# Performance work log

Measured on AMD Instinct MI355X. Metric: run time of the kernel, lower is better.

Reference implementation:

```python
import jax, jax.numpy as jnp
from jax import lax
import numpy as np

V = 50000          # num_word; embedding table has V+1 rows
D = 512            # embedding_dim / d_model
H = 8              # nhead
FF = 2048          # dim_feedforward (hidden_dim)
L = 32             # num_label (incl START/STOP)
START, STOP = L - 2, L - 1
S = 2048           # sentence length
NEG = -10000.0


def setup_inputs() -> dict:
    k = jax.random.split(jax.random.key(0), 10)
    def rn(key, shape, s=0.02):
        return jax.random.normal(key, shape, jnp.float32) * s
    transitions = jax.random.normal(k[8], (L, L), jnp.float32)
    transitions = transitions.at[START, :].set(NEG).at[:, STOP].set(NEG)
    return {
        "sentence": jax.random.randint(k[0], (S,), 0, V + 1),
        "embed": rn(k[1], (V + 1, D), 1.0),
        "Wqkv": rn(k[2], (3 * D, D)), "bqkv": jnp.zeros((3 * D,), jnp.float32),
        "Wo": rn(k[3], (D, D)), "bo": jnp.zeros((D,), jnp.float32),
        "ln1_g": jnp.ones((D,), jnp.float32), "ln1_b": jnp.zeros((D,), jnp.float32),
        "W1": rn(k[4], (FF, D)), "b1": jnp.zeros((FF,), jnp.float32),
        "W2": rn(k[5], (D, FF)), "b2": jnp.zeros((D,), jnp.float32),
        "ln2_g": jnp.ones((D,), jnp.float32), "ln2_b": jnp.zeros((D,), jnp.float32),
        "Wt": rn(k[6], (L, D)), "bt": jnp.zeros((L,), jnp.float32),
        "transitions": transitions,
    }


def _ln(x, g, b):
    m = jnp.mean(x, -1, keepdims=True)
    v = jnp.var(x, -1, keepdims=True)
    return (x - m) * lax.rsqrt(v + 1e-5) * g + b


def _transformer_feats(sentence, embed, Wqkv, bqkv, Wo, bo, ln1_g, ln1_b,
                       W1, b1, W2, b2, ln2_g, ln2_b, Wt, bt):
    x = embed[sentence]                                   # [S, D]
    qkv = x @ Wqkv.T + bqkv                               # [S, 3D]
    q, k, v = jnp.split(qkv, 3, axis=-1)
    to_heads = lambda t: t.reshape(S, H, D // H).transpose(1, 0, 2)  # [H, S, dh]
    q, k, v = to_heads(q), to_heads(k), to_heads(v)
    att = jax.nn.softmax(jnp.einsum('hsd,htd->hst', q, k) / np.float32(np.sqrt(D // H)), axis=-1)
    o = jnp.einsum('hst,htd->hsd', att, v).transpose(1, 0, 2).reshape(S, D)
    # post-norm TransformerEncoderLayer (eval mode: dropout off), relu FFN
    x = _ln(x + o @ Wo.T + bo, ln1_g, ln1_b)
    ff = jax.nn.relu(x @ W1.T + b1) @ W2.T + b2
    x = _ln(x + ff, ln2_g, ln2_b)
    return x @ Wt.T + bt                                  # [S, L] emission scores


def _viterbi(feats, transitions):
    init = jnp.full((L,), NEG, jnp.float32).at[START].set(0.0)
    def step(prev, emit):
        scores = prev[None, :] + transitions              # [next_tag, prev_tag]
        bp = jnp.argmax(scores, axis=1)                   # best prev tag per next tag
        return jnp.max(scores, axis=1) + emit, bp
    last, bps = lax.scan(step, init, feats)               # bps: [S, L]
    terminal = last + transitions[STOP]
    best = jnp.argmax(terminal)
    def back(tag, bp):
        return bp[tag], tag
    _, path = lax.scan(back, best, bps, reverse=True)     # path[t] = best tag at step t
    return terminal[best], path


def reference(sentence, embed, Wqkv, bqkv, Wo, bo, ln1_g, ln1_b,
              W1, b1, W2, b2, ln2_g, ln2_b, Wt, bt, transitions):
    feats = _transformer_feats(sentence, embed, Wqkv, bqkv, Wo, bo, ln1_g, ln1_b,
                               W1, b1, W2, b2, ln2_g, ln2_b, Wt, bt)
    score, path = _viterbi(feats, transitions)
    return score, path
```

## Files before the change

kernel.cpp:

```cpp
#include <hip/hip_runtime.h>
#include <cstddef>

#define S_LEN 2048
#define D_MODEL 512
#define NHEAD 8
#define DH 64
#define FF_DIM 2048
#define L_TAGS 32
#define START_TAG 30
#define STOP_TAG 31
#define NEGV (-10000.0f)

typedef unsigned int uint2v __attribute__((ext_vector_type(2)));
typedef __attribute__((ext_vector_type(8))) short short8v;
typedef __attribute__((ext_vector_type(4))) float f32x4;

union U8 { uint4 u; short8v s; };

__device__ __forceinline__ unsigned short f2bf(float f) {
  unsigned u = __float_as_uint(f);
  u += 0x7fff + ((u >> 16) & 1);
  return (unsigned short)(u >> 16);
}
__device__ __forceinline__ unsigned cvtpk(float lo, float hi) {
  unsigned r;
  asm("v_cvt_pk_bf16_f32 %0, %1, %2" : "=v"(r) : "v"(lo), "v"(hi));
  return r;
}

__global__ __launch_bounds__(256) void k_f2h4(const float* __restrict__ s0, short* __restrict__ d0,
                                              const float* __restrict__ s1, short* __restrict__ d1,
                                              const float* __restrict__ s2, short* __restrict__ d2,
                                              const float* __restrict__ s3, short* __restrict__ d3) {
  const int b = blockIdx.x;
  const float* src; short* dst; int i;
  if (b < 384)       { src = s0; dst = d0; i = b * 256 + threadIdx.x; }
  else if (b < 512)  { src = s1; dst = d1; i = (b - 384) * 256 + threadIdx.x; }
  else if (b < 1024) { src = s2; dst = d2; i = (b - 512) * 256 + threadIdx.x; }
  else               { src = s3; dst = d3; i = (b - 1024) * 256 + threadIdx.x; }
  f32x4 a = *(const f32x4*)(src + (size_t)i * 8);
  f32x4 c = *(const f32x4*)(src + (size_t)i * 8 + 4);
  U8 t;
  t.u.x = cvtpk(a[0], a[1]); t.u.y = cvtpk(a[2], a[3]);
  t.u.z = cvtpk(c[0], c[1]); t.u.w = cvtpk(c[2], c[3]);
  *(short8v*)(dst + (size_t)i * 8) = t.s;
}

__global__ __launch_bounds__(256, 2) void k_gemm_qkv(const int* __restrict__ sent,
                                                     const float* __restrict__ embed,
                                                     const short* __restrict__ B,
                                                     const float* __restrict__ bias,
                                                     short* __restrict__ C,
                                                     int N, int K) {
  __shared__ __align__(16) short As[2][128 * 64];
  __shared__ __align__(16) short Bs[2][128 * 64];
  const int tid = threadIdx.x;
  const int bm = blockIdx.y * 128, bn = blockIdx.x * 128;
  const int w = tid >> 6, lane = tid & 63;
  const int wr = w >> 1, wc = w & 1;
  const int fr = lane & 15, kg = lane >> 4;
  const int srow = tid >> 1, sc0 = (tid & 1) * 4;
  const int swz = srow & 7;
  const float* gA = embed + (size_t)sent[bm + srow] * K + sc0 * 8;
  const short* gB = B + (size_t)(bn + srow) * K + sc0 * 8;
  f32x4 ra[8];
  short8v rb[4];
  f32x4 acc[4][4] = {};

  auto loadg = [&](int k0) {
#pragma unroll
    for (int c = 0; c < 4; ++c) {
      ra[2 * c] = *(const f32x4*)(gA + k0 + c * 8);
      ra[2 * c + 1] = *(const f32x4*)(gA + k0 + c * 8 + 4);
      rb[c] = *(const short8v*)(gB + k0 + c * 8);
    }
  };
  auto storeb = [&](int b) {
    short* dA = &As[b][srow * 64];
    short* dB = &Bs[b][srow * 64];
#pragma unroll
    for (int c = 0; c < 4; ++c) {
      U8 ta;
      ta.u.x = cvtpk(ra[2 * c][0], ra[2 * c][1]);
      ta.u.y = cvtpk(ra[2 * c][2], ra[2 * c][3]);
      ta.u.z = cvtpk(ra[2 * c + 1][0], ra[2 * c + 1][1]);
      ta.u.w = cvtpk(ra[2 * c + 1][2], ra[2 * c + 1][3]);
      *(short8v*)(dA + (((sc0 + c) ^ swz) << 3)) = ta.s;
      *(short8v*)(dB + (((sc0 + c) ^ swz) << 3)) = rb[c];
    }
  };

  loadg(0);
  storeb(0);
  __syncthreads();
  int cur = 0;
  const int fswz = fr & 7;
  for (int k0 = 0; k0 < K; k0 += 64) {
    const bool more = (k0 + 64) < K;
    if (more) loadg(k0 + 64);
    const short* rA = &As[cur][(wr * 64 + fr) * 64];
    const short* rB = &Bs[cur][(wc * 64 + fr) * 64];
#pragma unroll
    for (int ks = 0; ks < 2; ++ks) {
      const int co = ((ks * 4 + kg) ^ fswz) << 3;
      short8v af[4], bf[4];
#pragma unroll
      for (int rt = 0; rt < 4; ++rt) af[rt] = *(const short8v*)(rA + rt * 16 * 64 + co);
#pragma unroll
      for (int ct = 0; ct < 4; ++ct) bf[ct] = *(const short8v*)(rB + ct * 16 * 64 + co);
#pragma unroll
      for (int rt = 0; rt < 4; ++rt)
#pragma unroll
        for (int ct = 0; ct < 4; ++ct)
          acc[rt][ct] = __builtin_amdgcn_mfma_f32_16x16x32_bf16(af[rt], bf[ct], acc[rt][ct], 0, 0, 0);
    }
    if (more) storeb(cur ^ 1);
    __syncthreads();
    cur ^= 1;
  }
#pragma unroll
  for (int rt = 0; rt < 4; ++rt) {
#pragma unroll
    for (int ct = 0; ct < 4; ++ct) {
      f32x4 v = acc[rt][ct];
      const int row0 = bm + wr * 64 + rt * 16 + kg * 4;
      const int col = bn + wc * 64 + ct * 16 + fr;
      const float bs = bias[col];
#pragma unroll
      for (int j = 0; j < 4; ++j)
        C[(size_t)(row0 + j) * N + col] = (short)f2bf(v[j] + bs);
    }
  }
}

template <int RT, bool RELU, bool OBF>
__global__ __launch_bounds__(256, 2) void k_gemm_bf(const short* __restrict__ A,
                                                    const short* __restrict__ B,
                                                    const float* __restrict__ bias,
                                                    void* __restrict__ Cp,
                                                    int M, int N, int K) {
  constexpr int BM = RT * 32;
  constexpr int CH = (BM * 8) / 256;
  __shared__ __align__(16) short As[2][BM * 64];
  __shared__ __align__(16) short Bs[2][BM * 64];
  const int tid = threadIdx.x;
  const int bm = blockIdx.y * BM, bn = blockIdx.x * BM;
  const int w = tid >> 6, lane = tid & 63;
  const int wr = w >> 1, wc = w & 1;
  const int fr = lane & 15, kg = lane >> 4;
  const int srow = (RT == 4) ? (tid >> 1) : (tid >> 2);
  const int sc0 = (RT == 4) ? ((tid & 1) * 4) : ((tid & 3) * 2);
  const int swz = srow & 7;
  const short* gA = A + (size_t)(bm + srow) * K + sc0 * 8;
  const short* gB = B + (size_t)(bn + srow) * K + sc0 * 8;
  short8v ra[CH], rb[CH];
  f32x4 acc[RT][RT] = {};

  auto loadg = [&](int k0) {
#pragma unroll
    for (int c = 0; c < CH; ++c) {
      ra[c] = *(const short8v*)(gA + k0 + c * 8);
      rb[c] = *(const short8v*)(gB + k0 + c * 8);
    }
  };
  auto storeb = [&](int b) {
    short* dA = &As[b][srow * 64];
    short* dB = &Bs[b][srow * 64];
#pragma unroll
    for (int c = 0; c < CH; ++c) {
      *(short8v*)(dA + (((sc0 + c) ^ swz) << 3)) = ra[c];
      *(short8v*)(dB + (((sc0 + c) ^ swz) << 3)) = rb[c];
    }
  };

  loadg(0);
  storeb(0);
  __syncthreads();
  int cur = 0;
  const int fswz = fr & 7;
  for (int k0 = 0; k0 < K; k0 += 64) {
    const bool more = (k0 + 64) < K;
    if (more) loadg(k0 + 64);
    const short* rA = &As[cur][(wr * (RT * 16) + fr) * 64];
    const short* rB = &Bs[cur][(wc * (RT * 16) + fr) * 64];
#pragma unroll
    for (int ks = 0; ks < 2; ++ks) {
      const int co = ((ks * 4 + kg) ^ fswz) << 3;
      short8v af[RT], bf[RT];
#pragma unroll
      for (int rt = 0; rt < RT; ++rt) af[rt] = *(const short8v*)(rA + rt * 16 * 64 + co);
#pragma unroll
      for (int ct = 0; ct < RT; ++ct) bf[ct] = *(const short8v*)(rB + ct * 16 * 64 + co);
#pragma unroll
      for (int rt = 0; rt < RT; ++rt)
#pragma unroll
        for (int ct = 0; ct < RT; ++ct)
          acc[rt][ct] = __builtin_amdgcn_mfma_f32_16x16x32_bf16(af[rt], bf[ct], acc[rt][ct], 0, 0, 0);
    }
    if (more) storeb(cur ^ 1);
    __syncthreads();
    cur ^= 1;
  }
#pragma unroll
  for (int rt = 0; rt < RT; ++rt) {
#pragma unroll
    for (int ct = 0; ct < RT; ++ct) {
      f32x4 v = acc[rt][ct];
      const int row0 = bm + wr * (RT * 16) + rt * 16 + kg * 4;
      const int col = bn + wc * (RT * 16) + ct * 16 + fr;
      const float bs = bias[col];
#pragma unroll
      for (int j = 0; j < 4; ++j) {
        float o = v[j] + bs;
        if (RELU) o = fmaxf(o, 0.f);
        if (OBF)
          ((short*)Cp)[(size_t)(row0 + j) * N + col] = (short)f2bf(o);
        else
          ((float*)Cp)[(size_t)(row0 + j) * N + col] = o;
      }
    }
  }
}

__global__ __launch_bounds__(256) void k_attn(const short* __restrict__ qkv,
                                              short* __restrict__ ob) {
  __shared__ __align__(16) short Ks[2][64 * 64];
  __shared__ __align__(16) short Vt[2][64 * 72];
  __shared__ __align__(16) short Pl[4][16 * 72];
  const int tid = threadIdx.x;
  const int b = blockIdx.x;
  const int h = b & 7;
  const int bq = (b >> 3) * 64;
  const int wq = tid >> 6, lane = tid & 63;
  const int fr = lane & 15, kg = lane >> 4;
  short8v qf[2];
  {
    const short* qsrc = qkv + (size_t)(bq + wq * 16 + fr) * 1536 + h * DH;
    qf[0] = *(const short8v*)(qsrc + kg * 8);
    qf[1] = *(const short8v*)(qsrc + 32 + kg * 8);
  }
  float m[4], l[4];
  f32x4 oac[4] = {};
#pragma unroll
  for (int j = 0; j < 4; ++j) { m[j] = -1e30f; l[j] = 0.f; }

  const int srow = tid >> 2, sc0 = (tid & 3) * 2;
  const int kpair = tid & 31, dgrp = tid >> 5;
  short8v kr0, kr1, va, vb;
  auto loadt = [&](int kt) {
    const short* kbase = qkv + (size_t)(kt * 64 + srow) * 1536 + 512 + h * DH;
    kr0 = *(const short8v*)(kbase + sc0 * 8);
    kr1 = *(const short8v*)(kbase + sc0 * 8 + 8);
    const short* vbase = qkv + (size_t)(kt * 64 + 2 * kpair) * 1536 + 1024 + h * DH + dgrp * 8;
    va = *(const short8v*)(vbase);
    vb = *(const short8v*)(vbase + 1536);
  };
  auto storet = [&](int cu) {
    short* dk = &Ks[cu][srow * 64];
    *(short8v*)(dk + ((sc0 ^ (srow & 7)) << 3)) = kr0;
    *(short8v*)(dk + (((sc0 + 1) ^ (srow & 7)) << 3)) = kr1;
#pragma unroll
    for (int i = 0; i < 8; ++i) {
      unsigned u = ((unsigned)(unsigned short)va[i]) |
                   (((unsigned)(unsigned short)vb[i]) << 16);
      *(unsigned*)&Vt[cu][(dgrp * 8 + i) * 72 + 2 * kpair] = u;
    }
  };

  loadt(0);
  int cur = 0;
  for (int kt = 0; kt < 32; ++kt) {
    storet(cur);
    __syncthreads();
    if (kt < 31) loadt(kt + 1);
    f32x4 sac[4] = {};
#pragma unroll
    for (int ks = 0; ks < 2; ++ks) {
#pragma unroll
      for (int ct = 0; ct < 4; ++ct) {
        const int row = ct * 16 + fr;
        short8v bfr = *(const short8v*)&Ks[cur][row * 64 + (((ks * 4 + kg) ^ (row & 7)) << 3)];
        sac[ct] = __builtin_amdgcn_mfma_f32_16x16x32_bf16(qf[ks], bfr, sac[ct], 0, 0, 0);
      }
    }
#pragma unroll
    for (int ct = 0; ct < 4; ++ct) sac[ct] *= 0.125f;
    float pv[4][4];
#pragma unroll
    for (int j = 0; j < 4; ++j) {
      float v = fmaxf(fmaxf(sac[0][j], sac[1][j]), fmaxf(sac[2][j], sac[3][j]));
#pragma unroll
      for (int off = 1; off < 16; off <<= 1) v = fmaxf(v, __shfl_xor(v, off, 64));
      float mn = fmaxf(m[j], v);
      float f = __expf(m[j] - mn);
      m[j] = mn;
      float rs = 0.f;
#pragma unroll
      for (int ct = 0; ct < 4; ++ct) {
        pv[ct][j] = __expf(sac[ct][j] - mn);
        rs += pv[ct][j];
      }
#pragma unroll
      for (int off = 1; off < 16; off <<= 1) rs += __shfl_xor(rs, off, 64);
      l[j] = l[j] * f + rs;
#pragma unroll
      for (int ct = 0; ct < 4; ++ct) oac[ct][j] *= f;
    }
#pragma unroll
    for (int ct = 0; ct < 4; ++ct)
#pragma unroll
      for (int j = 0; j < 4; ++j)
        Pl[wq][(kg * 4 + j) * 72 + ct * 16 + fr] = (short)f2bf(pv[ct][j]);
#pragma unroll
    for (int ks = 0; ks < 2; ++ks) {
      short8v paf = *(const short8v*)&Pl[wq][fr * 72 + ks * 32 + kg * 8];
#pragma unroll
      for (int ct = 0; ct < 4; ++ct) {
        short8v vf = *(const short8v*)&Vt[cur][(ct * 16 + fr) * 72 + ks * 32 + kg * 8];
        oac[ct] = __builtin_amdgcn_mfma_f32_16x16x32_bf16(paf, vf, oac[ct], 0, 0, 0);
      }
    }
    cur ^= 1;
  }
#pragma unroll
  for (int j = 0; j < 4; ++j) {
    float inv = 1.f / l[j];
    const int q = bq + wq * 16 + kg * 4 + j;
#pragma unroll
    for (int ct = 0; ct < 4; ++ct)
      ob[(size_t)q * D_MODEL + h * DH + ct * 16 + fr] = (short)f2bf(oac[ct][j] * inv);
  }
}

__global__ __launch_bounds__(128) void k_ln(const float* __restrict__ a,
                                            const int* __restrict__ sent,
                                            const float* __restrict__ embed,
                                            const float* __restrict__ r,
                                            const float* __restrict__ g,
                                            const float* __restrict__ b,
                                            float* __restrict__ out,
                                            short* __restrict__ outh) {
  __shared__ float red[2];
  const int row = blockIdx.x, tid = threadIdx.x;
  const size_t off = (size_t)row * D_MODEL + tid * 4;
  float4 av;
  if (sent)
    av = *(const float4*)(embed + (size_t)sent[row] * D_MODEL + tid * 4);
  else
    av = *(const float4*)(a + off);
  float4 rv = *(const float4*)(r + off);
  float v0 = av.x + rv.x, v1 = av.y + rv.y, v2 = av.z + rv.z, v3 = av.w + rv.w;
  float s = v0 + v1 + v2 + v3;
#pragma unroll
  for (int d = 1; d < 64; d <<= 1) s += __shfl_xor(s, d, 64);
  if ((tid & 63) == 0) red[tid >> 6] = s;
  __syncthreads();
  float mean = (red[0] + red[1]) * (1.f / 512.f);
  __syncthreads();
  float d0 = v0 - mean, d1 = v1 - mean, d2 = v2 - mean, d3 = v3 - mean;
  float sq = d0 * d0 + d1 * d1 + d2 * d2 + d3 * d3;
#pragma unroll
  for (int d = 1; d < 64; d <<= 1) sq += __shfl_xor(sq, d, 64);
  if ((tid & 63) == 0) red[tid >> 6] = sq;
  __syncthreads();
  float inv = rsqrtf((red[0] + red[1]) * (1.f / 512.f) + 1e-5f);
  float4 gv = *(const float4*)(g + tid * 4);
  float4 bv = *(const float4*)(b + tid * 4);
  float4 o;
  o.x = d0 * inv * gv.x + bv.x;
  o.y = d1 * inv * gv.y + bv.y;
  o.z = d2 * inv * gv.z + bv.z;
  o.w = d3 * inv * gv.w + bv.w;
  *(float4*)(out + off) = o;
  if (outh) {
    uint2v t;
    t[0] = cvtpk(o.x, o.y);
    t[1] = cvtpk(o.z, o.w);
    *(uint2v*)(outh + off) = t;
  }
}

__global__ __launch_bounds__(256) void k_feats(const float* __restrict__ x2,
                                               const float* __restrict__ Wt,
                                               const float* __restrict__ bt,
                                               float* __restrict__ feats) {
  const int tid = threadIdx.x;
  const int s = blockIdx.x * 8 + (tid >> 5);
  const int l = tid & 31;
  const float* xr = x2 + (size_t)s * D_MODEL;
  const float* wr = Wt + (size_t)l * D_MODEL;
  float acc = 0.f;
#pragma unroll 8
  for (int k = 0; k < D_MODEL; k += 4) {
    float4 xv = *(const float4*)(xr + k);
    float4 wv = *(const float4*)(wr + k);
    acc += xv.x * wv.x + xv.y * wv.y + xv.z * wv.z + xv.w * wv.w;
  }
  feats[s * L_TAGS + l] = acc + bt[l];
}

__global__ __launch_bounds__(64) void k_scan1(const float* __restrict__ feats,
                                              const float* __restrict__ T,
                                              float* __restrict__ P) {
  __shared__ float S[2][32];
  const int c = blockIdx.x >> 4;
  const int l = threadIdx.x;
  const int n = l & 31, pl = l >> 5;
  const int p = (blockIdx.x & 15) * 2 + pl;
  float Trow[32];
#pragma unroll
  for (int q = 0; q < 32; ++q) Trow[q] = T[n * 32 + q];
  const int tbase = c * 32;
  float er[4];
#pragma unroll
  for (int i = 0; i < 4; ++i) er[i] = feats[(tbase + i) * 32 + n];
  float a = T[n * 32 + p] + er[0];
  S[pl][n] = a;
  const float* fp = feats + (size_t)(tbase + 4) * 32 + n;
  er[0] = fp[0]; fp += 32;
  for (int u = 1; u < 32; ++u) {
    float e = er[u & 3];
    float enew = fp[0]; fp += 32;
    const float4* Sv = (const float4*)&S[pl][0];
    float g[32];
#pragma unroll
    for (int j4 = 0; j4 < 8; ++j4) {
      float4 sv = Sv[j4];
      g[j4 * 4 + 0] = sv.x + Trow[j4 * 4 + 0];
      g[j4 * 4 + 1] = sv.y + Trow[j4 * 4 + 1];
      g[j4 * 4 + 2] = sv.z + Trow[j4 * 4 + 2];
      g[j4 * 4 + 3] = sv.w + Trow[j4 * 4 + 3];
    }
#pragma unroll
    for (int st = 1; st < 32; st <<= 1)
#pragma unroll
      for (int j = 0; j < 32; j += 2 * st) g[j] = fmaxf(g[j], g[j + st]);
    a = g[0] + e;
    S[pl][n] = a;
    er[u & 3] = enew;
  }
  P[(size_t)c * 1024 + n * 32 + p] = a;
}

__global__ __launch_bounds__(64) void k_scan2(const float* __restrict__ P,
                                              const float* __restrict__ T,
                                              float* __restrict__ alphas,
                                              float* __restrict__ out,
                                              int* __restrict__ bestp) {
  __shared__ float Sa[32];
  const int l = threadIdx.x, n = l & 31, half = l >> 5;
  float a = (n == START_TAG) ? 0.f : NEGV;
  const float* pbase = P + n * 32 + half * 16;
  float4 pr[4];
#pragma unroll
  for (int j = 0; j < 4; ++j) pr[j] = *(const float4*)(pbase + j * 4);
  for (int c = 0; c < 64; ++c) {
    float4 nx[4];
#pragma unroll
    for (int j = 0; j < 4; ++j)
      nx[j] = *(const float4*)(pbase + (size_t)(c + 1) * 1024 + j * 4);
    alphas[(size_t)(c * 32) * 32 + n] = a;
    Sa[n] = a;
    const float4* Sv = (const float4*)&Sa[half * 16];
    float g[16];
#pragma unroll
    for (int j = 0; j < 4; ++j) {
      float4 sv = Sv[j];
      g[j * 4 + 0] = pr[j].x + sv.x;
      g[j * 4 + 1] = pr[j].y + sv.y;
      g[j * 4 + 2] = pr[j].z + sv.z;
      g[j * 4 + 3] = pr[j].w + sv.w;
    }
#pragma unroll
    for (int st = 1; st < 16; st <<= 1)
#pragma unroll
      for (int j = 0; j < 16; j += 2 * st) g[j] = fmaxf(g[j], g[j + st]);
    uint2v r = __builtin_amdgcn_permlane32_swap(__float_as_uint(g[0]),
                                                __float_as_uint(g[0]), false, false);
    a = fmaxf(__uint_as_float(r[0]), __uint_as_float(r[1]));
#pragma unroll
    for (int j = 0; j < 4; ++j) pr[j] = nx[j];
  }
  float term = a + T[STOP_TAG * 32 + n];
  float bv = term;
  int bi = n;
#pragma unroll
  for (int d = 1; d < 32; d <<= 1) {
    float ov = __shfl_xor(bv, d, 64);
    int oi = __shfl_xor(bi, d, 64);
    if (ov > bv || (ov == bv && oi < bi)) { bv = ov; bi = oi; }
  }
  if (l == 0) { out[0] = bv; *bestp = bi; }
}

__global__ __launch_bounds__(64) void k_scan3(const float* __restrict__ feats,
                                              const float* __restrict__ T,
                                              const float* __restrict__ alphas,
                                              unsigned char* __restrict__ cand,
                                              unsigned char* __restrict__ amap) {
  __shared__ float Sa[32];
  __shared__ unsigned char bpl[32][32];
  __shared__ unsigned cnd[256];
  const int c = blockIdx.x, l = threadIdx.x, n = l & 31, half = l >> 5;
  float Tr[16];
#pragma unroll
  for (int j = 0; j < 16; ++j) Tr[j] = T[n * 32 + half * 16 + j];
  const int tbase = c * 32;
  float a = alphas[(size_t)tbase * 32 + n];
  float er[4];
#pragma unroll
  for (int i = 0; i < 4; ++i) er[i] = feats[(tbase + i) * 32 + n];
  const float* fp = feats + (size_t)(tbase + 4) * 32 + n;
  Sa[n] = a;
  for (int u = 0; u < 32; ++u) {
    float e = er[u & 3];
    float enew = fp[0]; fp += 32;
    const float4* Sv = (const float4*)&Sa[half * 16];
    float4 s0 = Sv[0], s1 = Sv[1], s2 = Sv[2], s3 = Sv[3];
    float v[16] = {s0.x + Tr[0],  s0.y + Tr[1],  s0.z + Tr[2],  s0.w + Tr[3],
                   s1.x + Tr[4],  s1.y + Tr[5],  s1.z + Tr[6],  s1.w + Tr[7],
                   s2.x + Tr[8],  s2.y + Tr[9],  s2.z + Tr[10], s2.w + Tr[11],
                   s3.x + Tr[12], s3.y + Tr[13], s3.z + Tr[14], s3.w + Tr[15]};
    int id[16];
#pragma unroll
    for (int j = 0; j < 16; ++j) id[j] = half * 16 + j;
#pragma unroll
    for (int st = 1; st < 16; st <<= 1)
#pragma unroll
      for (int j = 0; j < 16; j += 2 * st)
        if (v[j + st] > v[j]) { v[j] = v[j + st]; id[j] = id[j + st]; }
    uint2v rv = __builtin_amdgcn_permlane32_swap(__float_as_uint(v[0]),
                                                 __float_as_uint(v[0]), false, false);
    uint2v ri = __builtin_amdgcn_permlane32_swap((unsigned)id[0], (unsigned)id[0],
                                                 false, false);
    float v0 = __uint_as_float(rv[0]), v1 = __uint_as_float(rv[1]);
    int i0 = (int)ri[0], i1 = (int)ri[1];
    float wv = (v1 > v0) ? v1 : v0;
    int wi = (v1 > v0) ? i1 : i0;
    bpl[u][n] = (unsigned char)wi;
    a = wv + e;
    Sa[n] = a;
    er[u & 3] = enew;
  }
  unsigned char* cnb = (unsigned char*)cnd;
  int tg = n;
  cnb[n * 32 + 31] = (unsigned char)n;
  for (int j = 31; j >= 1; --j) {
    tg = bpl[j][tg];
    cnb[n * 32 + (j - 1)] = (unsigned char)tg;
  }
  if (half == 0) amap[c * 32 + n] = bpl[0][tg];
#pragma unroll
  for (int i = 0; i < 4; ++i)
    ((unsigned*)(cand + (size_t)c * 1024))[l * 4 + i] = cnd[l * 4 + i];
}

__global__ __launch_bounds__(256) void k_trace2(const unsigned char* __restrict__ amap,
                                                const unsigned char* __restrict__ cand,
                                                const int* __restrict__ bestp,
                                                float* __restrict__ outp) {
  __shared__ unsigned char Am[64][32];
  __shared__ unsigned char et[64];
  const int tid = threadIdx.x;
  ((unsigned*)&Am[0][0])[tid] = ((const unsigned*)amap)[tid];
  ((unsigned*)&Am[32][0])[tid] = ((const unsigned*)amap)[tid + 256];
  __syncthreads();
  for (int d = 1; d < 64; d <<= 1) {
    unsigned char tmpv[8];
#pragma unroll
    for (int i = 0; i < 8; ++i) {
      int id = tid + 256 * i;
      int cc = id >> 5, e = id & 31;
      tmpv[i] = (cc + d < 64) ? Am[cc][Am[cc + d][e]] : Am[cc][e];
    }
    __syncthreads();
#pragma unroll
    for (int i = 0; i < 8; ++i) {
      int id = tid + 256 * i;
      Am[id >> 5][id & 31] = tmpv[i];
    }
    __syncthreads();
  }
  const int best = *bestp;
  if (tid < 64) et[tid] = (tid == 63) ? (unsigned char)best : Am[tid + 1][best];
  __syncthreads();
#pragma unroll
  for (int i = 0; i < 8; ++i) {
    int t = tid + 256 * i;
    int cc = t >> 5, j = t & 31;
    outp[1 + t] = (float)cand[(size_t)cc * 1024 + (size_t)et[cc] * 32 + j];
  }
}

extern "C" void kernel_launch(void* const* d_in, const int* in_sizes, int n_in,
                              void* d_out, int out_size, void* d_ws, size_t ws_size,
                              hipStream_t stream) {
  (void)in_sizes; (void)n_in; (void)out_size; (void)ws_size;
  const int* sent = (const int*)d_in[0];
  const float* embed = (const float*)d_in[1];
  const float* Wqkv = (const float*)d_in[2];
  const float* bqkv = (const float*)d_in[3];
  const float* Wo = (const float*)d_in[4];
  const float* bo = (const float*)d_in[5];
  const float* g1 = (const float*)d_in[6];
  const float* b1n = (const float*)d_in[7];
  const float* W1 = (const float*)d_in[8];
  const float* b1f = (const float*)d_in[9];
  const float* W2 = (const float*)d_in[10];
  const float* b2f = (const float*)d_in[11];
  const float* g2 = (const float*)d_in[12];
  const float* b2n = (const float*)d_in[13];
  const float* Wt = (const float*)d_in[14];
  const float* bt = (const float*)d_in[15];
  const float* T = (const float*)d_in[16];
  float* out = (float*)d_out;

  float* ws = (float*)d_ws;
  const size_t M1 = 1u << 20;
  short* qkvh = (short*)ws;
  short* obh = (short*)(ws + 2 * M1);
  float* yb = ws + 3 * M1;
  float* x1 = ws + 4 * M1;
  short* x1h = (short*)(ws + 5 * M1);
  short* ffbh = (short*)(ws + 6 * M1);
  float* zb = ws + 8 * M1;
  float* x2 = ws + 9 * M1;
  short* wqkvh = (short*)(ws + 10 * M1);
  short* woh = wqkvh + 786432;
  short* w1h = woh + 262144;
  short* w2h = w1h + 1048576;
  float* feats = ws + 11 * M1;
  float* alphas = feats + 2048 * 32 + 64;
  float* P = alphas + 2049 * 32 + 64;
  int* bestp = (int*)(P + 65 * 1024 + 64);
  unsigned char* cand = (unsigned char*)(bestp + 64);
  unsigned char* amap = cand + 2048 * 32;

  k_f2h4<<<dim3(1536), dim3(256), 0, stream>>>(Wqkv, wqkvh, Wo, woh, W1, w1h, W2, w2h);
  k_gemm_qkv<<<dim3(12, 16), dim3(256), 0, stream>>>(sent, embed, wqkvh, bqkv, qkvh, 1536, 512);
  k_attn<<<dim3(256), dim3(256), 0, stream>>>(qkvh, obh);
  k_gemm_bf<2, false, false><<<dim3(8, 32), dim3(256), 0, stream>>>(obh, woh, bo, yb, 2048, 512, 512);
  k_ln<<<dim3(2048), dim3(128), 0, stream>>>(nullptr, sent, embed, yb, g1, b1n, x1, x1h);
  k_gemm_bf<4, true, true><<<dim3(16, 16), dim3(256), 0, stream>>>(x1h, w1h, b1f, ffbh, 2048, 2048, 512);
  k_gemm_bf<2, false, false><<<dim3(8, 32), dim3(256), 0, stream>>>(ffbh, w2h, b2f, zb, 2048, 512, 2048);
  k_ln<<<dim3(2048), dim3(128), 0, stream>>>(x1, nullptr, nullptr, zb, g2, b2n, x2, (short*)nullptr);
  k_feats<<<dim3(256), dim3(256), 0, stream>>>(x2, Wt, bt, feats);
  k_scan1<<<dim3(1024), dim3(64), 0, stream>>>(feats, T, P);
  k_scan2<<<dim3(1), dim3(64), 0, stream>>>(P, T, alphas, out, bestp);
  k_scan3<<<dim3(64), dim3(64), 0, stream>>>(feats, T, alphas, cand, amap);
  k_trace2<<<dim3(1), dim3(256), 0, stream>>>(amap, cand, bestp, out);
}
```

Before: 187.3 us.

## Fuse final layernorm with emission projection, remap GEMM tiles, fold softmax scale into Q

Merges the second layernorm and the tag projection into one kernel, so the normalized x2 buffer is never written to or reread from global memory and one launch disappears. GEMM workgroups are remapped to interleave tiles across 8 groups, likely to spread them across XCDs for better cache locality. Attention pre-scales Q by 1/sqrt(dh)*log2(e) in bf16 and uses exp2, which removes the per-score multiply but adds one extra bf16 rounding of Q.

```diff
diff --git a/kernel.cpp b/kernel.cpp
--- a/kernel.cpp
+++ b/kernel.cpp
@@ -10,6 +10,7 @@
 #define START_TAG 30
 #define STOP_TAG 31
 #define NEGV (-10000.0f)
+#define QSCALE 0.18033688f
 
 typedef unsigned int uint2v __attribute__((ext_vector_type(2)));
 typedef __attribute__((ext_vector_type(8))) short short8v;
@@ -55,7 +56,11 @@
   __shared__ __align__(16) short As[2][128 * 64];
   __shared__ __align__(16) short Bs[2][128 * 64];
   const int tid = threadIdx.x;
-  const int bm = blockIdx.y * 128, bn = blockIdx.x * 128;
+  const int nwg = gridDim.x * gridDim.y;
+  int lin = blockIdx.x + gridDim.x * blockIdx.y;
+  int wk = (lin & 7) * (nwg >> 3) + (lin >> 3);
+  const int bxs = wk % gridDim.x, bys = wk / gridDim.x;
+  const int bm = bys * 128, bn = bxs * 128;
   const int w = tid >> 6, lane = tid & 63;
   const int wr = w >> 1, wc = w & 1;
   const int fr = lane & 15, kg = lane >> 4;
@@ -144,7 +149,11 @@
   __shared__ __align__(16) short As[2][BM * 64];
   __shared__ __align__(16) short Bs[2][BM * 64];
   const int tid = threadIdx.x;
-  const int bm = blockIdx.y * BM, bn = blockIdx.x * BM;
+  const int nwg = gridDim.x * gridDim.y;
+  int lin = blockIdx.x + gridDim.x * blockIdx.y;
+  int wk = (lin & 7) * (nwg >> 3) + (lin >> 3);
+  const int bxs = wk % gridDim.x, bys = wk / gridDim.x;
+  const int bm = bys * BM, bn = bxs * BM;
   const int w = tid >> 6, lane = tid & 63;
   const int wr = w >> 1, wc = w & 1;
   const int fr = lane & 15, kg = lane >> 4;
@@ -233,11 +242,23 @@
   const int bq = (b >> 3) * 64;
   const int wq = tid >> 6, lane = tid & 63;
   const int fr = lane & 15, kg = lane >> 4;
+  auto scale8 = [](short8v q) -> short8v {
+    unsigned wv[4];
+#pragma unroll
+    for (int i = 0; i < 4; ++i) {
+      float lo = __uint_as_float(((unsigned)(unsigned short)q[2 * i]) << 16) * QSCALE;
+      float hi = __uint_as_float(((unsigned)(unsigned short)q[2 * i + 1]) << 16) * QSCALE;
+      wv[i] = cvtpk(lo, hi);
+    }
+    U8 t;
+    t.u.x = wv[0]; t.u.y = wv[1]; t.u.z = wv[2]; t.u.w = wv[3];
+    return t.s;
+  };
   short8v qf[2];
   {
     const short* qsrc = qkv + (size_t)(bq + wq * 16 + fr) * 1536 + h * DH;
-    qf[0] = *(const short8v*)(qsrc + kg * 8);
-    qf[1] = *(const short8v*)(qsrc + 32 + kg * 8);
+    qf[0] = scale8(*(const short8v*)(qsrc + kg * 8));
+    qf[1] = scale8(*(const short8v*)(qsrc + 32 + kg * 8));
   }
   float m[4], l[4];
   f32x4 oac[4] = {};
@@ -283,8 +304,6 @@
         sac[ct] = __builtin_amdgcn_mfma_f32_16x16x32_bf16(qf[ks], bfr, sac[ct], 0, 0, 0);
       }
     }
-#pragma unroll
-    for (int ct = 0; ct < 4; ++ct) sac[ct] *= 0.125f;
     float pv[4][4];
 #pragma unroll
     for (int j = 0; j < 4; ++j) {
@@ -292,12 +311,12 @@
 #pragma unroll
       for (int off = 1; off < 16; off <<= 1) v = fmaxf(v, __shfl_xor(v, off, 64));
       float mn = fmaxf(m[j], v);
-      float f = __expf(m[j] - mn);
+      float f = __builtin_amdgcn_exp2f(m[j] - mn);
       m[j] = mn;
       float rs = 0.f;
 #pragma unroll
       for (int ct = 0; ct < 4; ++ct) {
-        pv[ct][j] = __expf(sac[ct][j] - mn);
+        pv[ct][j] = __builtin_amdgcn_exp2f(sac[ct][j] - mn);
         rs += pv[ct][j];
       }
 #pragma unroll
@@ -380,23 +399,52 @@
   }
 }
 
-__global__ __launch_bounds__(256) void k_feats(const float* __restrict__ x2,
-                                               const float* __restrict__ Wt,
-                                               const float* __restrict__ bt,
-                                               float* __restrict__ feats) {
-  const int tid = threadIdx.x;
-  const int s = blockIdx.x * 8 + (tid >> 5);
-  const int l = tid & 31;
-  const float* xr = x2 + (size_t)s * D_MODEL;
-  const float* wr = Wt + (size_t)l * D_MODEL;
-  float acc = 0.f;
-#pragma unroll 8
-  for (int k = 0; k < D_MODEL; k += 4) {
-    float4 xv = *(const float4*)(xr + k);
-    float4 wv = *(const float4*)(wr + k);
-    acc += xv.x * wv.x + xv.y * wv.y + xv.z * wv.z + xv.w * wv.w;
-  }
-  feats[s * L_TAGS + l] = acc + bt[l];
+__global__ __launch_bounds__(128) void k_lnfeats(const float* __restrict__ a,
+                                                 const float* __restrict__ r,
+                                                 const float* __restrict__ g,
+                                                 const float* __restrict__ b,
+                                                 const float* __restrict__ Wt,
+                                                 const float* __restrict__ bt,
+                                                 float* __restrict__ feats) {
+  __shared__ float red[2];
+  __shared__ float part[2][32];
+  const int row = blockIdx.x, tid = threadIdx.x;
+  const size_t off = (size_t)row * D_MODEL + tid * 4;
+  float4 av = *(const float4*)(a + off);
+  float4 rv = *(const float4*)(r + off);
+  float v0 = av.x + rv.x, v1 = av.y + rv.y, v2 = av.z + rv.z, v3 = av.w + rv.w;
+  float s = v0 + v1 + v2 + v3;
+#pragma unroll
+  for (int d = 1; d < 64; d <<= 1) s += __shfl_xor(s, d, 64);
+  if ((tid & 63) == 0) red[tid >> 6] = s;
+  __syncthreads();
+  float mean = (red[0] + red[1]) * (1.f / 512.f);
+  __syncthreads();
+  float d0 = v0 - mean, d1 = v1 - mean, d2 = v2 - mean, d3 = v3 - mean;
+  float sq = d0 * d0 + d1 * d1 + d2 * d2 + d3 * d3;
+#pragma unroll
+  for (int d = 1; d < 64; d <<= 1) sq += __shfl_xor(sq, d, 64);
+  if ((tid & 63) == 0) red[tid >> 6] = sq;
+  __syncthreads();
+  float inv = rsqrtf((red[0] + red[1]) * (1.f / 512.f) + 1e-5f);
+  float4 gv = *(const float4*)(g + tid * 4);
+  float4 bv = *(const float4*)(b + tid * 4);
+  float4 o;
+  o.x = d0 * inv * gv.x + bv.x;
+  o.y = d1 * inv * gv.y + bv.y;
+  o.z = d2 * inv * gv.z + bv.z;
+  o.w = d3 * inv * gv.w + bv.w;
+  const int lane = tid & 63, wv = tid >> 6;
+#pragma unroll
+  for (int l = 0; l < 32; ++l) {
+    float4 wr4 = *(const float4*)(Wt + (size_t)l * D_MODEL + tid * 4);
+    float p = o.x * wr4.x + o.y * wr4.y + o.z * wr4.z + o.w * wr4.w;
+#pragma unroll
+    for (int d = 1; d < 64; d <<= 1) p += __shfl_xor(p, d, 64);
+    if (lane == 0) part[wv][l] = p;
+  }
+  __syncthreads();
+  if (tid < 32) feats[(size_t)row * L_TAGS + tid] = part[0][tid] + part[1][tid] + bt[tid];
 }
 
 __global__ __launch_bounds__(64) void k_scan1(const float* __restrict__ feats,
@@ -535,10 +583,10 @@
                                                  false, false);
     float v0 = __uint_as_float(rv[0]), v1 = __uint_as_float(rv[1]);
     int i0 = (int)ri[0], i1 = (int)ri[1];
-    float wv = (v1 > v0) ? v1 : v0;
+    float wvv = (v1 > v0) ? v1 : v0;
     int wi = (v1 > v0) ? i1 : i0;
     bpl[u][n] = (unsigned char)wi;
-    a = wv + e;
+    a = wvv + e;
     Sa[n] = a;
     er[u & 3] = enew;
   }
@@ -624,7 +672,6 @@
   short* x1h = (short*)(ws + 5 * M1);
   short* ffbh = (short*)(ws + 6 * M1);
   float* zb = ws + 8 * M1;
-  float* x2 = ws + 9 * M1;
   short* wqkvh = (short*)(ws + 10 * M1);
   short* woh = wqkvh + 786432;
   short* w1h = woh + 262144;
@@ -643,8 +690,7 @@
   k_ln<<<dim3(2048), dim3(128), 0, stream>>>(nullptr, sent, embed, yb, g1, b1n, x1, x1h);
   k_gemm_bf<4, true, true><<<dim3(16, 16), dim3(256), 0, stream>>>(x1h, w1h, b1f, ffbh, 2048, 2048, 512);
   k_gemm_bf<2, false, false><<<dim3(8, 32), dim3(256), 0, stream>>>(ffbh, w2h, b2f, zb, 2048, 512, 2048);
-  k_ln<<<dim3(2048), dim3(128), 0, stream>>>(x1, nullptr, nullptr, zb, g2, b2n, x2, (short*)nullptr);
-  k_feats<<<dim3(256), dim3(256), 0, stream>>>(x2, Wt, bt, feats);
+  k_lnfeats<<<dim3(2048), dim3(128), 0, stream>>>(x1, zb, g2, b2n, Wt, bt, feats);
   k_scan1<<<dim3(1024), dim3(64), 0, stream>>>(feats, T, P);
   k_scan2<<<dim3(1), dim3(64), 0, stream>>>(P, T, alphas, out, bestp);
   k_scan3<<<dim3(64), dim3(64), 0, stream>>>(feats, T, alphas, cand, amap);
```

Measured after the change: 179.1 us. -4.4%, faster.
